# Performance work log

Measured on AMD Instinct MI355X. Metric: run time of the kernel, lower is better.

## Reference

```python
import jax, jax.numpy as jnp
import numpy as np

NUM_EXPERTS = 8
TOP_K = 2

def setup_inputs() -> dict:
    key = jax.random.key(0)
    ks = jax.random.split(key, 5)
    B, S, D, F, E = 4, 2048, 1024, 4096, NUM_EXPERTS
    x = jax.random.normal(ks[0], (B, S, D), dtype=jnp.float32)
    router_w = jax.random.normal(ks[1], (D, E), dtype=jnp.float32) * 0.02
    router_b = jnp.zeros((E,), dtype=jnp.float32)
    w1 = jax.random.normal(ks[2], (E, D, F), dtype=jnp.float32) * 0.02
    b1 = jnp.zeros((E, F), dtype=jnp.float32)
    w2 = jax.random.normal(ks[3], (E, F, D), dtype=jnp.float32) * 0.02
    b2 = jnp.zeros((E, D), dtype=jnp.float32)
    return {"x": x, "router_w": router_w, "router_b": router_b,
            "w1": w1, "b1": b1, "w2": w2, "b2": b2}

def reference(x, router_w, router_b, w1, b1, w2, b2):
    B, S, D = x.shape
    E = router_w.shape[1]
    x_flat = x.reshape(-1, D)                                  # [N, D]
    router_probs = jax.nn.softmax(x_flat @ router_w + router_b, axis=-1)  # [N, E]
    topk_probs, topk_idx = jax.lax.top_k(router_probs, TOP_K)  # [N, K]
    topk_probs = topk_probs / jnp.sum(topk_probs, axis=-1, keepdims=True)
    # combine weight per (token, expert): sum over top-k slots assigned to that expert
    cw = jnp.sum(topk_probs[..., None] * jax.nn.one_hot(topk_idx, E, dtype=x.dtype), axis=1)  # [N, E]
    out = jnp.zeros_like(x_flat)
    for e in range(E):  # small fixed expert count; each iter is a dense GEMM pair
        h = jax.nn.gelu(x_flat @ w1[e] + b1[e], approximate=False)  # [N, F]
        out = out + cw[:, e:e + 1] * (h @ w2[e] + b2[e])            # [N, D]
    return out.reshape(B, S, D)
```

## Files before the change

### kernel.cpp

```cpp
#include <hip/hip_runtime.h>
#include <hip/hip_bf16.h>

typedef __attribute__((ext_vector_type(8))) __bf16 bf16x8;
typedef __attribute__((ext_vector_type(4))) float f32x4;

#define NTOK 8192
#define D_DIM 1024
#define F_DIM 4096
#define NEXP 8
#define SLOT_TOT 16384
#define SLOT_CAP 16640

__device__ __forceinline__ unsigned short f2b(float f) {
  __hip_bfloat16 b = __float2bfloat16(f);
  return reinterpret_cast<unsigned short&>(b);
}

__device__ __forceinline__ void gload_lds16(const void* g, void* l) {
  __builtin_amdgcn_global_load_lds(
      (__attribute__((address_space(1))) void*)g,
      (__attribute__((address_space(3))) void*)l, 16, 0, 0);
}


__global__ void init_counts_kernel(int* counts) {
  if (threadIdx.x < NEXP) counts[threadIdx.x] = 0;
}

__global__ void zero_out_kernel(float* out) {
  const int i = blockIdx.x * 256 + threadIdx.x;
  reinterpret_cast<float4*>(out)[i] = make_float4(0.f, 0.f, 0.f, 0.f);
}

__global__ void convert_x_kernel(const float* __restrict__ x,
                                 __hip_bfloat16* __restrict__ xb) {
  const int i = (blockIdx.x * 256 + threadIdx.x) * 4;
  const float4 v = *reinterpret_cast<const float4*>(x + i);
  union { unsigned short u[4]; uint2 d; } o;
  o.u[0] = f2b(v.x); o.u[1] = f2b(v.y); o.u[2] = f2b(v.z); o.u[3] = f2b(v.w);
  *reinterpret_cast<uint2*>(xb + i) = o.d;
}

__global__ void transpose_conv_kernel(const float* __restrict__ src,
                                      __hip_bfloat16* __restrict__ dst,
                                      int R, int C) {
  __shared__ float tile[64][65];
  const int e = blockIdx.z;
  src += (size_t)e * R * C;
  dst += (size_t)e * R * C;
  const int c0 = blockIdx.x * 64, r0 = blockIdx.y * 64;
  const int tx = threadIdx.x, ty = threadIdx.y;
  #pragma unroll
  for (int j = 0; j < 4; ++j) {
    const float4 v = *reinterpret_cast<const float4*>(
        &src[(size_t)(r0 + ty + j * 16) * C + c0 + tx * 4]);
    tile[ty + j * 16][tx * 4 + 0] = v.x;
    tile[ty + j * 16][tx * 4 + 1] = v.y;
    tile[ty + j * 16][tx * 4 + 2] = v.z;
    tile[ty + j * 16][tx * 4 + 3] = v.w;
  }
  __syncthreads();
  #pragma unroll
  for (int j = 0; j < 4; ++j) {
    const int c = ty + j * 16;
    union { unsigned short u[4]; uint2 d; } o;
    #pragma unroll
    for (int i = 0; i < 4; ++i) o.u[i] = f2b(tile[tx * 4 + i][c]);
    *reinterpret_cast<uint2*>(&dst[(size_t)(c0 + c) * R + r0 + tx * 4]) = o.d;
  }
}

__global__ void router_kernel(const float* __restrict__ x,
                              const float* __restrict__ rw,
                              const float* __restrict__ rb,
                              int* __restrict__ topk_idx,
                              float* __restrict__ topk_w,
                              int* __restrict__ counts) {
  __shared__ float rwT[NEXP * D_DIM];
  const int tid = threadIdx.x;
  for (int i = tid; i < NEXP * D_DIM; i += 256) {
    const int d = i >> 3, e = i & 7;
    rwT[e * D_DIM + d] = rw[i];
  }
  __syncthreads();

  const int wave = tid >> 6, lane = tid & 63;
  const int tok = blockIdx.x * 4 + wave;
  const float* xr = x + (size_t)tok * D_DIM;

  float acc[NEXP];
  #pragma unroll
  for (int e = 0; e < NEXP; ++e) acc[e] = 0.f;

  for (int i = 0; i < D_DIM / 64; ++i) {
    const int d = i * 64 + lane;
    const float xv = xr[d];
    #pragma unroll
    for (int e = 0; e < NEXP; ++e) acc[e] += xv * rwT[e * D_DIM + d];
  }
  #pragma unroll
  for (int off = 32; off > 0; off >>= 1) {
    #pragma unroll
    for (int e = 0; e < NEXP; ++e) acc[e] += __shfl_xor(acc[e], off);
  }

  if (lane == 0) {
    float l[NEXP];
    #pragma unroll
    for (int e = 0; e < NEXP; ++e) l[e] = acc[e] + rb[e];
    int i1 = 0;
    #pragma unroll
    for (int e = 1; e < NEXP; ++e) if (l[e] > l[i1]) i1 = e;
    int i2 = (i1 == 0) ? 1 : 0;
    #pragma unroll
    for (int e = 0; e < NEXP; ++e) if (e != i1 && e != i2 && l[e] > l[i2]) i2 = e;
    const float w1 = 1.f / (1.f + __expf(l[i2] - l[i1]));
    topk_idx[tok * 2 + 0] = i1;
    topk_idx[tok * 2 + 1] = i2;
    topk_w[tok * 2 + 0] = w1;
    topk_w[tok * 2 + 1] = 1.f - w1;
    atomicAdd(&counts[i1], 1);
    atomicAdd(&counts[i2], 1);
  }
}

__global__ void offsets_kernel(const int* __restrict__ counts,
                               int* __restrict__ offsets,
                               int* __restrict__ cursors,
                               int* __restrict__ slot_token,
                               float* __restrict__ slot_cw) {
  const int t = threadIdx.x;
  if (t == 0) {
    int s = 0;
    for (int e = 0; e < NEXP; ++e) { offsets[e] = s; cursors[e] = s; s += counts[e]; }
    offsets[NEXP] = s;
  }
  if (t < SLOT_CAP - SLOT_TOT) {
    slot_token[SLOT_TOT + t] = 0;
    slot_cw[SLOT_TOT + t] = 0.f;
  }
}

__global__ void scatter_kernel(const int* __restrict__ topk_idx,
                               const float* __restrict__ topk_w,
                               int* __restrict__ cursors,
                               int* __restrict__ slot_token,
                               float* __restrict__ slot_cw) {
  const int tok = blockIdx.x * 256 + threadIdx.x;
  if (tok >= NTOK) return;
  #pragma unroll
  for (int k = 0; k < 2; ++k) {
    const int e = topk_idx[tok * 2 + k];
    const int p = atomicAdd(&cursors[e], 1);
    slot_token[p] = tok;
    slot_cw[p] = topk_w[tok * 2 + k];
  }
}

template <int PHASE>
__global__ __launch_bounds__(512, 4) void moe_gemm(
    const __hip_bfloat16* __restrict__ A,
    const __hip_bfloat16* __restrict__ B,
    const float* __restrict__ bias,
    const int* __restrict__ slot_token,
    const float* __restrict__ slot_cw,
    const int* __restrict__ counts,
    const int* __restrict__ offsets,
    __hip_bfloat16* __restrict__ Hout,
    float* __restrict__ Out) {
  constexpr int K = (PHASE == 1) ? D_DIM : F_DIM;
  constexpr int NCOL = (PHASE == 1) ? F_DIM : D_DIM;
  constexpr int KT = K / 32;

  const int e = blockIdx.z;
  const int cnt = counts[e];
  const int mt = blockIdx.y;
  if (mt * 256 >= cnt) return;
  const int nt = blockIdx.x;
  const int base = offsets[e];

  __shared__ unsigned short lA[3][8192];
  __shared__ unsigned short lB[3][4096];

  const int tid = threadIdx.x;
  const int w = tid >> 6, lane = tid & 63;
  const int r = lane & 15, kg = lane >> 4;
  const int wm = w >> 1, wn = w & 1;

  const int rowA0 = mt * 256 + w * 16 + r;
  const int rowA1 = mt * 256 + (w + 8) * 16 + r;
  const __hip_bfloat16 *gA0, *gA1;
  if constexpr (PHASE == 1) {
    gA0 = A + (size_t)slot_token[base + rowA0] * K + kg * 8;
    gA1 = A + (size_t)slot_token[base + rowA1] * K + kg * 8;
  } else {
    gA0 = A + (size_t)(base + rowA0) * K + kg * 8;
    gA1 = A + (size_t)(base + rowA1) * K + kg * 8;
  }
  const __hip_bfloat16* Be = B + (size_t)e * NCOL * K;
  const __hip_bfloat16* gB0 = Be + (size_t)(nt * 128 + w * 16 + r) * K + kg * 8;

  f32x4 acc[4][4] = {};

  auto stage = [&](unsigned short* pa, unsigned short* pb) {
    gload_lds16(gA0, pa + w * 512);
    gload_lds16(gA1, pa + (w + 8) * 512);
    gload_lds16(gB0, pb + w * 512);
    gA0 += 32; gA1 += 32; gB0 += 32;
  };
  auto compute = [&](const unsigned short* pa, const unsigned short* pb) {
    bf16x8 af[4], bfr[4];
    #pragma unroll
    for (int i = 0; i < 4; ++i) {
      af[i]  = *(const bf16x8*)(pa + (wm * 4 + i) * 512 + lane * 8);
      bfr[i] = *(const bf16x8*)(pb + (wn * 4 + i) * 512 + lane * 8);
    }
    #pragma unroll
    for (int mi = 0; mi < 4; ++mi)
      #pragma unroll
      for (int ni = 0; ni < 4; ++ni)
        acc[mi][ni] = __builtin_amdgcn_mfma_f32_16x16x32_bf16(
            af[mi], bfr[ni], acc[mi][ni], 0, 0, 0);
  };

  unsigned short *pa0 = lA[0], *pa1 = lA[1], *pa2 = lA[2];
  unsigned short *pb0 = lB[0], *pb1 = lB[1], *pb2 = lB[2];

  stage(pa0, pb0);
  stage(pa1, pb1);
  stage(pa2, pb2);

  for (int t = 0; t < KT - 3; ++t) {
    asm volatile("s_waitcnt vmcnt(6)" ::: "memory");
    __builtin_amdgcn_sched_barrier(0);
    __builtin_amdgcn_s_barrier();
    __builtin_amdgcn_sched_barrier(0);
    compute(pa0, pb0);
    __builtin_amdgcn_sched_barrier(0);
    __builtin_amdgcn_s_barrier();
    __builtin_amdgcn_sched_barrier(0);
    stage(pa0, pb0);
    unsigned short* ta = pa0; pa0 = pa1; pa1 = pa2; pa2 = ta;
    unsigned short* tb = pb0; pb0 = pb1; pb1 = pb2; pb2 = tb;
  }
  asm volatile("s_waitcnt vmcnt(6)" ::: "memory");
  __builtin_amdgcn_sched_barrier(0);
  __builtin_amdgcn_s_barrier();
  __builtin_amdgcn_sched_barrier(0);
  compute(pa0, pb0);
  asm volatile("s_waitcnt vmcnt(3)" ::: "memory");
  __builtin_amdgcn_sched_barrier(0);
  __builtin_amdgcn_s_barrier();
  __builtin_amdgcn_sched_barrier(0);
  compute(pa1, pb1);
  asm volatile("s_waitcnt vmcnt(0)" ::: "memory");
  __builtin_amdgcn_sched_barrier(0);
  __builtin_amdgcn_s_barrier();
  __builtin_amdgcn_sched_barrier(0);
  compute(pa2, pb2);

  const int rem = cnt - mt * 256;
  const int q4 = (lane >> 4) * 4;

  if constexpr (PHASE == 1) {
    #pragma unroll
    for (int ni = 0; ni < 4; ++ni) {
      const int col = nt * 128 + wn * 64 + ni * 16 + (lane & 15);
      const float bv = bias[e * NCOL + col];
      #pragma unroll
      for (int mi = 0; mi < 4; ++mi) {
        #pragma unroll
        for (int rr = 0; rr < 4; ++rr) {
          const int rloc = wm * 64 + mi * 16 + q4 + rr;
          if (rloc < rem) {
            float v = acc[mi][ni][rr] + bv;
            v = 0.5f * v * (1.f + erff(v * 0.70710678118654752f));
            Hout[(size_t)(base + mt * 256 + rloc) * F_DIM + col] = __float2bfloat16(v);
          }
        }
      }
    }
  } else {
    #pragma unroll
    for (int mi = 0; mi < 4; ++mi) {
      int toks[4]; float cws[4];
      #pragma unroll
      for (int rr = 0; rr < 4; ++rr) {
        const int rloc = wm * 64 + mi * 16 + q4 + rr;
        const int slot = base + mt * 256 + rloc;
        const bool ok = (rloc < rem);
        toks[rr] = ok ? slot_token[slot] : -1;
        cws[rr]  = ok ? slot_cw[slot] : 0.f;
      }
      #pragma unroll
      for (int ni = 0; ni < 4; ++ni) {
        const int col = nt * 128 + wn * 64 + ni * 16 + (lane & 15);
        const float bv = bias[e * NCOL + col];
        #pragma unroll
        for (int rr = 0; rr < 4; ++rr) {
          if (toks[rr] >= 0)
            atomicAdd(&Out[(size_t)toks[rr] * D_DIM + col], cws[rr] * (acc[mi][ni][rr] + bv));
        }
      }
    }
  }
}


extern "C" void kernel_launch(void* const* d_in, const int* in_sizes, int n_in,
                              void* d_out, int out_size, void* d_ws, size_t ws_size,
                              hipStream_t stream) {
  const float* x  = (const float*)d_in[0];
  const float* rw = (const float*)d_in[1];
  const float* rb = (const float*)d_in[2];
  const float* w1 = (const float*)d_in[3];
  const float* b1 = (const float*)d_in[4];
  const float* w2 = (const float*)d_in[5];
  const float* b2 = (const float*)d_in[6];
  float* out = (float*)d_out;

  char* p = (char*)d_ws;
  size_t used = 0;
  auto carve = [&](size_t bytes) {
    char* r = p + used;
    used += (bytes + 255) & ~(size_t)255;
    return (void*)r;
  };
  __hip_bfloat16* xb  = (__hip_bfloat16*)carve((size_t)NTOK * D_DIM * 2);
  __hip_bfloat16* w1t = (__hip_bfloat16*)carve((size_t)NEXP * F_DIM * D_DIM * 2);
  __hip_bfloat16* w2t = (__hip_bfloat16*)carve((size_t)NEXP * D_DIM * F_DIM * 2);
  __hip_bfloat16* h   = (__hip_bfloat16*)carve((size_t)SLOT_CAP * F_DIM * 2);
  int*   topk_idx   = (int*)carve((size_t)NTOK * 2 * 4);
  float* topk_w     = (float*)carve((size_t)NTOK * 2 * 4);
  int*   slot_token = (int*)carve((size_t)SLOT_CAP * 4);
  float* slot_cw    = (float*)carve((size_t)SLOT_CAP * 4);
  int* counts  = (int*)carve(256);
  int* offsets = (int*)carve(256);
  int* cursors = (int*)carve(256);

  zero_out_kernel<<<8192, 256, 0, stream>>>(out);
  if (used > ws_size) return;

  init_counts_kernel<<<1, 64, 0, stream>>>(counts);
  router_kernel<<<NTOK / 4, 256, 0, stream>>>(x, rw, rb, topk_idx, topk_w, counts);
  offsets_kernel<<<1, 256, 0, stream>>>(counts, offsets, cursors, slot_token, slot_cw);
  scatter_kernel<<<NTOK / 256, 256, 0, stream>>>(topk_idx, topk_w, cursors, slot_token, slot_cw);

  convert_x_kernel<<<(NTOK * D_DIM) / (256 * 4), 256, 0, stream>>>(x, xb);
  dim3 tb(16, 16);
  transpose_conv_kernel<<<dim3(F_DIM / 64, D_DIM / 64, NEXP), tb, 0, stream>>>(w1, w1t, D_DIM, F_DIM);
  transpose_conv_kernel<<<dim3(D_DIM / 64, F_DIM / 64, NEXP), tb, 0, stream>>>(w2, w2t, F_DIM, D_DIM);

  moe_gemm<1><<<dim3(F_DIM / 128, 32, NEXP), 512, 0, stream>>>(
      xb, w1t, b1, slot_token, slot_cw, counts, offsets, h, nullptr);
  moe_gemm<2><<<dim3(D_DIM / 128, 32, NEXP), 512, 0, stream>>>(
      h, w2t, b2, slot_token, slot_cw, counts, offsets, nullptr, out);
}
```

Baseline: 1.070 ms.

## Enlarge GEMM tiles to 256x256, pre-gather tokens, replace atomics with combine kernel

Expert activations are now gathered into a contiguous bf16 buffer in slot order before the first GEMM. Both GEMMs use 256x256 tiles with an 8x4 MFMA accumulator per wave and launch_bounds occupancy lowered to 2. The down-projection writes a bf16 per-slot output instead of atomically adding into the fp32 output, and a separate combine kernel sums the two slots per token. The aim is more data reuse per tile and no float atomics, at the cost of higher register/LDS pressure, an extra bf16 rounding of the expert outputs, and extra gather/combine passes.

Result: slower. 1.270 ms (+18.7%).

```diff
diff --git a/kernel.cpp b/kernel.cpp
--- a/kernel.cpp
+++ b/kernel.cpp
@@ -10,6 +10,7 @@
 #define NEXP 8
 #define SLOT_TOT 16384
 #define SLOT_CAP 16640
+#define MT_MAX 32
 
 __device__ __forceinline__ unsigned short f2b(float f) {
   __hip_bfloat16 b = __float2bfloat16(f);
@@ -32,13 +33,40 @@
   reinterpret_cast<float4*>(out)[i] = make_float4(0.f, 0.f, 0.f, 0.f);
 }
 
-__global__ void convert_x_kernel(const float* __restrict__ x,
-                                 __hip_bfloat16* __restrict__ xb) {
-  const int i = (blockIdx.x * 256 + threadIdx.x) * 4;
-  const float4 v = *reinterpret_cast<const float4*>(x + i);
-  union { unsigned short u[4]; uint2 d; } o;
+__global__ void gather_x_kernel(const float* __restrict__ x,
+                                const int* __restrict__ slot_token,
+                                __hip_bfloat16* __restrict__ xg) {
+  const int s = blockIdx.x;
+  const int t = slot_token[s];
+  const int d = threadIdx.x * 4;
+  const float4 v = *reinterpret_cast<const float4*>(x + (size_t)t * D_DIM + d);
+  union { unsigned short u[4]; uint2 q; } o;
   o.u[0] = f2b(v.x); o.u[1] = f2b(v.y); o.u[2] = f2b(v.z); o.u[3] = f2b(v.w);
-  *reinterpret_cast<uint2*>(xb + i) = o.d;
+  *reinterpret_cast<uint2*>(xg + (size_t)s * D_DIM + d) = o.q;
+}
+
+__global__ void combine_kernel(const __hip_bfloat16* __restrict__ ys,
+                               const int* __restrict__ slot_pos,
+                               const float* __restrict__ topk_w,
+                               float* __restrict__ out) {
+  const int tok = blockIdx.x;
+  const int d = threadIdx.x * 4;
+  const int s0 = slot_pos[tok * 2], s1 = slot_pos[tok * 2 + 1];
+  const float w0 = topk_w[tok * 2], w1 = topk_w[tok * 2 + 1];
+  union { unsigned short u[4]; uint2 q; } a, b;
+  a.q = *reinterpret_cast<const uint2*>(ys + (size_t)s0 * D_DIM + d);
+  b.q = *reinterpret_cast<const uint2*>(ys + (size_t)s1 * D_DIM + d);
+  float4 r;
+  const unsigned short* au = a.u; const unsigned short* bu = b.u;
+  float va[4];
+  #pragma unroll
+  for (int i = 0; i < 4; ++i) {
+    unsigned int ua = (unsigned int)au[i] << 16;
+    unsigned int ub = (unsigned int)bu[i] << 16;
+    va[i] = w0 * reinterpret_cast<float&>(ua) + w1 * reinterpret_cast<float&>(ub);
+  }
+  r.x = va[0]; r.y = va[1]; r.z = va[2]; r.w = va[3];
+  *reinterpret_cast<float4*>(out + (size_t)tok * D_DIM + d) = r;
 }
 
 __global__ void transpose_conv_kernel(const float* __restrict__ src,
@@ -127,8 +155,7 @@
 __global__ void offsets_kernel(const int* __restrict__ counts,
                                int* __restrict__ offsets,
                                int* __restrict__ cursors,
-                               int* __restrict__ slot_token,
-                               float* __restrict__ slot_cw) {
+                               int* __restrict__ slot_token) {
   const int t = threadIdx.x;
   if (t == 0) {
     int s = 0;
@@ -137,15 +164,13 @@
   }
   if (t < SLOT_CAP - SLOT_TOT) {
     slot_token[SLOT_TOT + t] = 0;
-    slot_cw[SLOT_TOT + t] = 0.f;
   }
 }
 
 __global__ void scatter_kernel(const int* __restrict__ topk_idx,
-                               const float* __restrict__ topk_w,
                                int* __restrict__ cursors,
                                int* __restrict__ slot_token,
-                               float* __restrict__ slot_cw) {
+                               int* __restrict__ slot_pos) {
   const int tok = blockIdx.x * 256 + threadIdx.x;
   if (tok >= NTOK) return;
   #pragma unroll
@@ -153,74 +178,67 @@
     const int e = topk_idx[tok * 2 + k];
     const int p = atomicAdd(&cursors[e], 1);
     slot_token[p] = tok;
-    slot_cw[p] = topk_w[tok * 2 + k];
+    slot_pos[tok * 2 + k] = p;
   }
 }
 
 template <int PHASE>
-__global__ __launch_bounds__(512, 4) void moe_gemm(
+__global__ __launch_bounds__(512, 2) void moe_gemm(
     const __hip_bfloat16* __restrict__ A,
     const __hip_bfloat16* __restrict__ B,
     const float* __restrict__ bias,
-    const int* __restrict__ slot_token,
-    const float* __restrict__ slot_cw,
     const int* __restrict__ counts,
     const int* __restrict__ offsets,
-    __hip_bfloat16* __restrict__ Hout,
-    float* __restrict__ Out) {
-  constexpr int K = (PHASE == 1) ? D_DIM : F_DIM;
+    __hip_bfloat16* __restrict__ Cout) {
+  constexpr int K    = (PHASE == 1) ? D_DIM : F_DIM;
   constexpr int NCOL = (PHASE == 1) ? F_DIM : D_DIM;
-  constexpr int KT = K / 32;
-
-  const int e = blockIdx.z;
+  constexpr int KT   = K / 32;
+
+  const int bid = blockIdx.x;
+  const int e = bid & 7;
+  const int i = bid >> 3;
+  const int mt = i & (MT_MAX - 1);
+  const int nt = i >> 5;
   const int cnt = counts[e];
-  const int mt = blockIdx.y;
   if (mt * 256 >= cnt) return;
-  const int nt = blockIdx.x;
   const int base = offsets[e];
 
   __shared__ unsigned short lA[3][8192];
-  __shared__ unsigned short lB[3][4096];
+  __shared__ unsigned short lB[3][8192];
 
   const int tid = threadIdx.x;
   const int w = tid >> 6, lane = tid & 63;
   const int r = lane & 15, kg = lane >> 4;
-  const int wm = w >> 1, wn = w & 1;
-
-  const int rowA0 = mt * 256 + w * 16 + r;
-  const int rowA1 = mt * 256 + (w + 8) * 16 + r;
-  const __hip_bfloat16 *gA0, *gA1;
-  if constexpr (PHASE == 1) {
-    gA0 = A + (size_t)slot_token[base + rowA0] * K + kg * 8;
-    gA1 = A + (size_t)slot_token[base + rowA1] * K + kg * 8;
-  } else {
-    gA0 = A + (size_t)(base + rowA0) * K + kg * 8;
-    gA1 = A + (size_t)(base + rowA1) * K + kg * 8;
-  }
-  const __hip_bfloat16* Be = B + (size_t)e * NCOL * K;
-  const __hip_bfloat16* gB0 = Be + (size_t)(nt * 128 + w * 16 + r) * K + kg * 8;
-
-  f32x4 acc[4][4] = {};
+  const int wm = w >> 2, wn = w & 3;
+
+  const __hip_bfloat16* gA0 = A + (size_t)(base + mt * 256 + w * 16 + r) * K + kg * 8;
+  const __hip_bfloat16* gA1 = gA0 + (size_t)128 * K;
+  const __hip_bfloat16* gB0 = B + ((size_t)e * NCOL + nt * 256 + w * 16 + r) * K + kg * 8;
+  const __hip_bfloat16* gB1 = gB0 + (size_t)128 * K;
+
+  f32x4 acc[8][4] = {};
 
   auto stage = [&](unsigned short* pa, unsigned short* pb) {
     gload_lds16(gA0, pa + w * 512);
     gload_lds16(gA1, pa + (w + 8) * 512);
     gload_lds16(gB0, pb + w * 512);
-    gA0 += 32; gA1 += 32; gB0 += 32;
+    gload_lds16(gB1, pb + (w + 8) * 512);
+    gA0 += 32; gA1 += 32; gB0 += 32; gB1 += 32;
   };
   auto compute = [&](const unsigned short* pa, const unsigned short* pb) {
-    bf16x8 af[4], bfr[4];
-    #pragma unroll
-    for (int i = 0; i < 4; ++i) {
-      af[i]  = *(const bf16x8*)(pa + (wm * 4 + i) * 512 + lane * 8);
-      bfr[i] = *(const bf16x8*)(pb + (wn * 4 + i) * 512 + lane * 8);
-    }
-    #pragma unroll
-    for (int mi = 0; mi < 4; ++mi)
+    bf16x8 af[8], bfr[4];
+    #pragma unroll
+    for (int m = 0; m < 8; ++m)
+      af[m] = *(const bf16x8*)(pa + (wm * 8 + m) * 512 + lane * 8);
+    #pragma unroll
+    for (int n = 0; n < 4; ++n)
+      bfr[n] = *(const bf16x8*)(pb + (wn * 4 + n) * 512 + lane * 8);
+    #pragma unroll
+    for (int m = 0; m < 8; ++m)
       #pragma unroll
-      for (int ni = 0; ni < 4; ++ni)
-        acc[mi][ni] = __builtin_amdgcn_mfma_f32_16x16x32_bf16(
-            af[mi], bfr[ni], acc[mi][ni], 0, 0, 0);
+      for (int n = 0; n < 4; ++n)
+        acc[m][n] = __builtin_amdgcn_mfma_f32_16x16x32_bf16(
+            af[m], bfr[n], acc[m][n], 0, 0, 0);
   };
 
   unsigned short *pa0 = lA[0], *pa1 = lA[1], *pa2 = lA[2];
@@ -231,7 +249,7 @@
   stage(pa2, pb2);
 
   for (int t = 0; t < KT - 3; ++t) {
-    asm volatile("s_waitcnt vmcnt(6)" ::: "memory");
+    asm volatile("s_waitcnt vmcnt(8)" ::: "memory");
     __builtin_amdgcn_sched_barrier(0);
     __builtin_amdgcn_s_barrier();
     __builtin_amdgcn_sched_barrier(0);
@@ -243,12 +261,12 @@
     unsigned short* ta = pa0; pa0 = pa1; pa1 = pa2; pa2 = ta;
     unsigned short* tb = pb0; pb0 = pb1; pb1 = pb2; pb2 = tb;
   }
-  asm volatile("s_waitcnt vmcnt(6)" ::: "memory");
+  asm volatile("s_waitcnt vmcnt(8)" ::: "memory");
   __builtin_amdgcn_sched_barrier(0);
   __builtin_amdgcn_s_barrier();
   __builtin_amdgcn_sched_barrier(0);
   compute(pa0, pb0);
-  asm volatile("s_waitcnt vmcnt(3)" ::: "memory");
+  asm volatile("s_waitcnt vmcnt(4)" ::: "memory");
   __builtin_amdgcn_sched_barrier(0);
   __builtin_amdgcn_s_barrier();
   __builtin_amdgcn_sched_barrier(0);
@@ -261,45 +279,22 @@
 
   const int rem = cnt - mt * 256;
   const int q4 = (lane >> 4) * 4;
-
-  if constexpr (PHASE == 1) {
-    #pragma unroll
-    for (int ni = 0; ni < 4; ++ni) {
-      const int col = nt * 128 + wn * 64 + ni * 16 + (lane & 15);
-      const float bv = bias[e * NCOL + col];
-      #pragma unroll
-      for (int mi = 0; mi < 4; ++mi) {
-        #pragma unroll
-        for (int rr = 0; rr < 4; ++rr) {
-          const int rloc = wm * 64 + mi * 16 + q4 + rr;
-          if (rloc < rem) {
-            float v = acc[mi][ni][rr] + bv;
-            v = 0.5f * v * (1.f + erff(v * 0.70710678118654752f));
-            Hout[(size_t)(base + mt * 256 + rloc) * F_DIM + col] = __float2bfloat16(v);
-          }
-        }
-      }
-    }
-  } else {
-    #pragma unroll
-    for (int mi = 0; mi < 4; ++mi) {
-      int toks[4]; float cws[4];
+  const int c15 = lane & 15;
+
+  #pragma unroll
+  for (int n = 0; n < 4; ++n) {
+    const int col = nt * 256 + wn * 64 + n * 16 + c15;
+    const float bv = bias[e * NCOL + col];
+    #pragma unroll
+    for (int m = 0; m < 8; ++m) {
       #pragma unroll
       for (int rr = 0; rr < 4; ++rr) {
-        const int rloc = wm * 64 + mi * 16 + q4 + rr;
-        const int slot = base + mt * 256 + rloc;
-        const bool ok = (rloc < rem);
-        toks[rr] = ok ? slot_token[slot] : -1;
-        cws[rr]  = ok ? slot_cw[slot] : 0.f;
-      }
-      #pragma unroll
-      for (int ni = 0; ni < 4; ++ni) {
-        const int col = nt * 128 + wn * 64 + ni * 16 + (lane & 15);
-        const float bv = bias[e * NCOL + col];
-        #pragma unroll
-        for (int rr = 0; rr < 4; ++rr) {
-          if (toks[rr] >= 0)
-            atomicAdd(&Out[(size_t)toks[rr] * D_DIM + col], cws[rr] * (acc[mi][ni][rr] + bv));
+        const int rloc = wm * 128 + m * 16 + q4 + rr;
+        if (rloc < rem) {
+          float v = acc[m][n][rr] + bv;
+          if constexpr (PHASE == 1)
+            v = 0.5f * v * (1.f + erff(v * 0.70710678118654752f));
+          Cout[(size_t)(base + mt * 256 + rloc) * NCOL + col] = __float2bfloat16(v);
         }
       }
     }
@@ -326,33 +321,38 @@
     used += (bytes + 255) & ~(size_t)255;
     return (void*)r;
   };
-  __hip_bfloat16* xb  = (__hip_bfloat16*)carve((size_t)NTOK * D_DIM * 2);
+  __hip_bfloat16* xg  = (__hip_bfloat16*)carve((size_t)SLOT_CAP * D_DIM * 2);
+  __hip_bfloat16* ys  = xg;
   __hip_bfloat16* w1t = (__hip_bfloat16*)carve((size_t)NEXP * F_DIM * D_DIM * 2);
   __hip_bfloat16* w2t = (__hip_bfloat16*)carve((size_t)NEXP * D_DIM * F_DIM * 2);
   __hip_bfloat16* h   = (__hip_bfloat16*)carve((size_t)SLOT_CAP * F_DIM * 2);
   int*   topk_idx   = (int*)carve((size_t)NTOK * 2 * 4);
   float* topk_w     = (float*)carve((size_t)NTOK * 2 * 4);
   int*   slot_token = (int*)carve((size_t)SLOT_CAP * 4);
-  float* slot_cw    = (float*)carve((size_t)SLOT_CAP * 4);
+  int*   slot_pos   = (int*)carve((size_t)NTOK * 2 * 4);
   int* counts  = (int*)carve(256);
   int* offsets = (int*)carve(256);
   int* cursors = (int*)carve(256);
 
-  zero_out_kernel<<<8192, 256, 0, stream>>>(out);
-  if (used > ws_size) return;
+  if (used > ws_size) {
+    zero_out_kernel<<<8192, 256, 0, stream>>>(out);
+    return;
+  }
 
   init_counts_kernel<<<1, 64, 0, stream>>>(counts);
   router_kernel<<<NTOK / 4, 256, 0, stream>>>(x, rw, rb, topk_idx, topk_w, counts);
-  offsets_kernel<<<1, 256, 0, stream>>>(counts, offsets, cursors, slot_token, slot_cw);
-  scatter_kernel<<<NTOK / 256, 256, 0, stream>>>(topk_idx, topk_w, cursors, slot_token, slot_cw);
-
-  convert_x_kernel<<<(NTOK * D_DIM) / (256 * 4), 256, 0, stream>>>(x, xb);
+  offsets_kernel<<<1, 256, 0, stream>>>(counts, offsets, cursors, slot_token);
+  scatter_kernel<<<NTOK / 256, 256, 0, stream>>>(topk_idx, cursors, slot_token, slot_pos);
+  gather_x_kernel<<<SLOT_CAP, 256, 0, stream>>>(x, slot_token, xg);
+
   dim3 tb(16, 16);
   transpose_conv_kernel<<<dim3(F_DIM / 64, D_DIM / 64, NEXP), tb, 0, stream>>>(w1, w1t, D_DIM, F_DIM);
   transpose_conv_kernel<<<dim3(D_DIM / 64, F_DIM / 64, NEXP), tb, 0, stream>>>(w2, w2t, F_DIM, D_DIM);
 
-  moe_gemm<1><<<dim3(F_DIM / 128, 32, NEXP), 512, 0, stream>>>(
-      xb, w1t, b1, slot_token, slot_cw, counts, offsets, h, nullptr);
-  moe_gemm<2><<<dim3(D_DIM / 128, 32, NEXP), 512, 0, stream>>>(
-      h, w2t, b2, slot_token, slot_cw, counts, offsets, nullptr, out);
-}
+  moe_gemm<1><<<NEXP * MT_MAX * (F_DIM / 256), 512, 0, stream>>>(
+      xg, w1t, b1, counts, offsets, h);
+  moe_gemm<2><<<NEXP * MT_MAX * (D_DIM / 256), 512, 0, stream>>>(
+      h, w2t, b2, counts, offsets, ys);
+
+  combine_kernel<<<NTOK, 256, 0, stream>>>(ys, slot_pos, topk_w, out);
+}
```
